# Optimization experiments

Measured on AMD Instinct MI355X. Metric: run time of the kernel, lower is better.

The kernel has to match this reference:

```python
import jax, jax.numpy as jnp
import numpy as np

INPUT_DIM = 512
HIDDEN_DIM = 512
T, B = 512, 128


def setup_inputs() -> dict:
    key = jax.random.key(0)
    ks = jax.random.split(key, 9)
    s_in = 1.0 / np.sqrt(INPUT_DIM + HIDDEN_DIM)
    d = INPUT_DIM + HIDDEN_DIM
    inputs = jax.random.normal(ks[0], (T, B, INPUT_DIM), dtype=jnp.float32)
    def lin(kw, kb):
        W = jax.random.uniform(kw, (HIDDEN_DIM, d), minval=-s_in, maxval=s_in, dtype=jnp.float32)
        b = jax.random.uniform(kb, (HIDDEN_DIM,), minval=-s_in, maxval=s_in, dtype=jnp.float32)
        return W, b
    Wf, bf = lin(ks[1], ks[2])
    Wi, bi = lin(ks[3], ks[4])
    Wg, bg = lin(ks[5], ks[6])
    Wo, bo = lin(ks[7], ks[8])
    return {"inputs": inputs, "Wf": Wf, "bf": bf, "Wi": Wi, "bi": bi,
            "Wg": Wg, "bg": bg, "Wo": Wo, "bo": bo}


def _lstm(inputs, Wf, bf, Wi, bi, Wg, bg, Wo, bo):
    B_ = inputs.shape[1]
    h0 = jnp.zeros((B_, HIDDEN_DIM), dtype=inputs.dtype)
    c0 = jnp.zeros((B_, HIDDEN_DIM), dtype=inputs.dtype)

    def step(carry, x):
        hx, cx = carry
        combined = jnp.concatenate([x, hx], axis=1)  # [B, input+hidden]
        f = jax.nn.sigmoid(combined @ Wf.T + bf)
        i = jax.nn.sigmoid(combined @ Wi.T + bi)
        g = jnp.tanh(combined @ Wg.T + bg)
        o = jax.nn.sigmoid(combined @ Wo.T + bo)
        cx = f * cx + i * g
        hx = o * jnp.tanh(cx)
        return (hx, cx), hx

    (hx, cx), outputs = jax.lax.scan(step, (h0, c0), inputs)
    return outputs, (hx, cx)


def reference(inputs, Wf, bf, Wi, bi, Wg, bg, Wo, bo):
    return _lstm(inputs, Wf, bf, Wi, bi, Wg, bg, Wo, bo)
```

## Files before the change

kernel.cpp:

```cpp
#include <hip/hip_runtime.h>
#include <stdint.h>

#define T_STEPS 512
#define BATCH   128
#define HID     512
#define KTOT    1024

typedef __attribute__((ext_vector_type(8))) short          bf16x8;
typedef __attribute__((ext_vector_type(8))) unsigned short u16x8;
typedef __attribute__((ext_vector_type(4))) float          f32x4;

__device__ inline unsigned short f2bf(float f) {
    union { float f; unsigned u; } x; x.f = f;
    unsigned r = x.u + 0x7FFFu + ((x.u >> 16) & 1u);
    return (unsigned short)(r >> 16);
}

__device__ inline float sigmoidf_(float x) { return 1.f / (1.f + __expf(-x)); }
__device__ inline float tanhf_(float x)    { float e = __expf(2.f * x); return 1.f - 2.f / (e + 1.f); }

__global__ void cast_x_kernel(const float* __restrict__ x, unsigned short* __restrict__ y, int n) {
    int i = (blockIdx.x * blockDim.x + threadIdx.x) * 8;
    if (i >= n) return;
    float4 a = *(const float4*)(x + i);
    float4 b = *(const float4*)(x + i + 4);
    u16x8 v;
    v[0] = f2bf(a.x); v[1] = f2bf(a.y); v[2] = f2bf(a.z); v[3] = f2bf(a.w);
    v[4] = f2bf(b.x); v[5] = f2bf(b.y); v[6] = f2bf(b.z); v[7] = f2bf(b.w);
    *(u16x8*)(y + i) = v;
}

__device__ inline void load_x32(const float* xf, const unsigned short* xbf, int use_xbf,
                                size_t off, uint4& a, uint4& b) {
    if (use_xbf) {
        const uint4* p = (const uint4*)(xbf + off);
        a = p[0]; b = p[1];
    } else {
        const float4* p = (const float4*)(xf + off);
        float4 f0 = p[0], f1 = p[1], f2 = p[2], f3 = p[3];
        u16x8 v;
        v[0] = f2bf(f0.x); v[1] = f2bf(f0.y); v[2] = f2bf(f0.z); v[3] = f2bf(f0.w);
        v[4] = f2bf(f1.x); v[5] = f2bf(f1.y); v[6] = f2bf(f1.z); v[7] = f2bf(f1.w);
        a = *(uint4*)&v;
        u16x8 w;
        w[0] = f2bf(f2.x); w[1] = f2bf(f2.y); w[2] = f2bf(f2.z); w[3] = f2bf(f2.w);
        w[4] = f2bf(f3.x); w[5] = f2bf(f3.y); w[6] = f2bf(f3.z); w[7] = f2bf(f3.w);
        b = *(uint4*)&w;
    }
}

__global__ __launch_bounds__(512, 2) void lstm_kernel(
    const float* __restrict__ xf,
    const unsigned short* __restrict__ xbf,
    const float* __restrict__ Wf, const float* __restrict__ bfv,
    const float* __restrict__ Wi, const float* __restrict__ biv,
    const float* __restrict__ Wg, const float* __restrict__ bgv,
    const float* __restrict__ Wo, const float* __restrict__ bov,
    float* __restrict__ out,
    unsigned int* __restrict__ flags,
    unsigned short* __restrict__ hbuf,
    int use_xbf)
{
    __shared__ __align__(16) unsigned short comb[16][1048];
    __shared__ float gp[4][4][16][34];

    const int tid  = threadIdx.x;
    const int bgc  = blockIdx.x >> 4;
    const int cg   = blockIdx.x & 15;
    const int w    = tid >> 6;
    const int lane = tid & 63;
    const int kh   = w & 3;
    const int uh   = w >> 2;
    const int n    = lane & 15;
    const int quad = lane >> 4;
    const int unit = cg * 32 + uh * 16 + n;

    bf16x8 wfr[4][8];
    {
        const float* Wptr[4] = {Wf, Wi, Wg, Wo};
#pragma unroll
        for (int g = 0; g < 4; ++g) {
            const float* wrow = Wptr[g] + (size_t)unit * KTOT;
#pragma unroll
            for (int j = 0; j < 8; ++j) {
                const int kk = (j < 4) ? (kh * 4 + j) : (16 + kh * 4 + (j - 4));
                const float4* p = (const float4*)(wrow + kk * 32 + quad * 8);
                float4 a = p[0], b = p[1];
                u16x8 v;
                v[0] = f2bf(a.x); v[1] = f2bf(a.y); v[2] = f2bf(a.z); v[3] = f2bf(a.w);
                v[4] = f2bf(b.x); v[5] = f2bf(b.y); v[6] = f2bf(b.z); v[7] = f2bf(b.w);
                wfr[g][j] = (bf16x8)v;
            }
        }
    }

    const int srow = tid >> 5;
    const int scol = tid & 31;

    const int bc = srow, uc = scol;
    float creg = 0.f;
    const int bglob = bgc * 16 + bc;
    const int uglob = cg * 32 + uc;
    const int bgrow = bgc * 16 + srow;

    float biasv[4];
    biasv[0] = bfv[uglob]; biasv[1] = biv[uglob];
    biasv[2] = bgv[uglob]; biasv[3] = bov[uglob];

    const size_t xstride = (size_t)HID;

    {
        uint4 a, b;
        load_x32(xf, xbf, use_xbf, ((size_t)(0 * BATCH + bgrow)) * xstride + scol * 16, a, b);
        *(uint4*)&comb[srow][scol * 16]     = a;
        *(uint4*)&comb[srow][scol * 16 + 8] = b;
        uint4 z = {0u, 0u, 0u, 0u};
        *(uint4*)&comb[srow][512 + scol * 16]     = z;
        *(uint4*)&comb[srow][512 + scol * 16 + 8] = z;
    }
    __syncthreads();

    f32x4 acc[4];
#pragma unroll
    for (int g = 0; g < 4; ++g) acc[g] = (f32x4){0.f, 0.f, 0.f, 0.f};
    {
        bf16x8 af[4];
#pragma unroll
        for (int j = 0; j < 4; ++j)
            af[j] = *(const bf16x8*)&comb[n][(kh * 4 + j) * 32 + quad * 8];
#pragma unroll
        for (int j = 0; j < 4; ++j)
#pragma unroll
            for (int g = 0; g < 4; ++g)
                acc[g] = __builtin_amdgcn_mfma_f32_16x16x32_bf16(af[j], wfr[g][j], acc[g], 0, 0, 0);
    }

    uint4 pfa, pfb;
    load_x32(xf, xbf, use_xbf, ((size_t)(1 * BATCH + bgrow)) * xstride + scol * 16, pfa, pfb);

    for (int t = 0; t < T_STEPS; ++t) {
        if (t > 0) {
            if (lane < 16) {
                unsigned int* fp = flags + ((size_t)(t - 1) * 8 + bgc) * 16 + lane;
                while (__hip_atomic_load(fp, __ATOMIC_RELAXED, __HIP_MEMORY_SCOPE_AGENT) == 0u) {}
            }
            const unsigned long long* src = (const unsigned long long*)
                (hbuf + (size_t)((t - 1) & 1) * BATCH * HID + (size_t)bgrow * HID + scol * 16);
            unsigned long long v0 = __hip_atomic_load(src + 0, __ATOMIC_RELAXED, __HIP_MEMORY_SCOPE_AGENT);
            unsigned long long v1 = __hip_atomic_load(src + 1, __ATOMIC_RELAXED, __HIP_MEMORY_SCOPE_AGENT);
            unsigned long long v2 = __hip_atomic_load(src + 2, __ATOMIC_RELAXED, __HIP_MEMORY_SCOPE_AGENT);
            unsigned long long v3 = __hip_atomic_load(src + 3, __ATOMIC_RELAXED, __HIP_MEMORY_SCOPE_AGENT);
            uint4 a, b;
            a.x = (unsigned)v0; a.y = (unsigned)(v0 >> 32);
            a.z = (unsigned)v1; a.w = (unsigned)(v1 >> 32);
            b.x = (unsigned)v2; b.y = (unsigned)(v2 >> 32);
            b.z = (unsigned)v3; b.w = (unsigned)(v3 >> 32);
            *(uint4*)&comb[srow][512 + scol * 16]     = a;
            *(uint4*)&comb[srow][512 + scol * 16 + 8] = b;
        }
        __syncthreads();

        {
            bf16x8 af[4];
#pragma unroll
            for (int j = 0; j < 4; ++j)
                af[j] = *(const bf16x8*)&comb[n][(16 + kh * 4 + j) * 32 + quad * 8];
#pragma unroll
            for (int j = 0; j < 4; ++j)
#pragma unroll
                for (int g = 0; g < 4; ++g)
                    acc[g] = __builtin_amdgcn_mfma_f32_16x16x32_bf16(af[j], wfr[g][4 + j], acc[g], 0, 0, 0);
        }

#pragma unroll
        for (int g = 0; g < 4; ++g)
#pragma unroll
            for (int r = 0; r < 4; ++r)
                gp[kh][g][quad * 4 + r][uh * 16 + n] = acc[g][r];
        if (t + 1 < T_STEPS) {
            *(uint4*)&comb[srow][scol * 16]     = pfa;
            *(uint4*)&comb[srow][scol * 16 + 8] = pfb;
        }
        __syncthreads();

        {
            float s0 = gp[0][0][bc][uc] + gp[1][0][bc][uc] + gp[2][0][bc][uc] + gp[3][0][bc][uc] + biasv[0];
            float s1 = gp[0][1][bc][uc] + gp[1][1][bc][uc] + gp[2][1][bc][uc] + gp[3][1][bc][uc] + biasv[1];
            float s2 = gp[0][2][bc][uc] + gp[1][2][bc][uc] + gp[2][2][bc][uc] + gp[3][2][bc][uc] + biasv[2];
            float s3 = gp[0][3][bc][uc] + gp[1][3][bc][uc] + gp[2][3][bc][uc] + gp[3][3][bc][uc] + biasv[3];
            float fv = sigmoidf_(s0);
            float iv = sigmoidf_(s1);
            float gv = tanhf_(s2);
            float ov = sigmoidf_(s3);
            float cn = fv * creg + iv * gv;
            creg = cn;
            float hv = ov * tanhf_(cn);
            unsigned int us  = (unsigned int)f2bf(hv);
            unsigned int us1 = (unsigned int)__shfl_down((int)us, 1);
            if ((uc & 1) == 0) {
                unsigned int pv = us | (us1 << 16);
                unsigned int* hp = (unsigned int*)(hbuf + (size_t)(t & 1) * BATCH * HID
                                                   + (size_t)bglob * HID + uglob);
                __hip_atomic_store(hp, pv, __ATOMIC_RELAXED, __HIP_MEMORY_SCOPE_AGENT);
            }
            out[(size_t)t * BATCH * HID + (size_t)bglob * HID + uglob] = hv;
            if (t == T_STEPS - 1) {
                out[(size_t)T_STEPS * BATCH * HID + (size_t)bglob * HID + uglob] = hv;
                out[(size_t)T_STEPS * BATCH * HID + BATCH * HID + (size_t)bglob * HID + uglob] = cn;
            }
        }

        if (t + 1 < T_STEPS) {
#pragma unroll
            for (int g = 0; g < 4; ++g) acc[g] = (f32x4){0.f, 0.f, 0.f, 0.f};
            bf16x8 af[4];
#pragma unroll
            for (int j = 0; j < 4; ++j)
                af[j] = *(const bf16x8*)&comb[n][(kh * 4 + j) * 32 + quad * 8];
#pragma unroll
            for (int j = 0; j < 4; ++j)
#pragma unroll
                for (int g = 0; g < 4; ++g)
                    acc[g] = __builtin_amdgcn_mfma_f32_16x16x32_bf16(af[j], wfr[g][j], acc[g], 0, 0, 0);
        }

        __builtin_amdgcn_s_waitcnt(0);
        __syncthreads();
        if (tid == 0) {
            __hip_atomic_store(flags + ((size_t)t * 8 + bgc) * 16 + cg, 1u,
                               __ATOMIC_RELAXED, __HIP_MEMORY_SCOPE_AGENT);
        }
        if (t + 2 < T_STEPS) {
            load_x32(xf, xbf, use_xbf,
                     ((size_t)((t + 2) * BATCH + bgrow)) * xstride + scol * 16, pfa, pfb);
        }
    }
}

extern "C" void kernel_launch(void* const* d_in, const int* in_sizes, int n_in,
                              void* d_out, int out_size, void* d_ws, size_t ws_size,
                              hipStream_t stream) {
    (void)in_sizes; (void)n_in; (void)out_size;
    const float* x   = (const float*)d_in[0];
    const float* Wf  = (const float*)d_in[1];
    const float* bfv = (const float*)d_in[2];
    const float* Wi  = (const float*)d_in[3];
    const float* biv = (const float*)d_in[4];
    const float* Wg  = (const float*)d_in[5];
    const float* bgv = (const float*)d_in[6];
    const float* Wo  = (const float*)d_in[7];
    const float* bov = (const float*)d_in[8];
    float* out = (float*)d_out;

    unsigned char* ws = (unsigned char*)d_ws;
    unsigned int*   flags = (unsigned int*)ws;
    unsigned short* hbuf  = (unsigned short*)(ws + 262144);
    unsigned short* xbf   = (unsigned short*)(ws + 524288);

    size_t need = 524288 + (size_t)T_STEPS * BATCH * HID * 2;
    int use_xbf = (ws_size >= need) ? 1 : 0;

    hipMemsetAsync(flags, 0, 262144, stream);
    if (use_xbf) {
        int nelem = T_STEPS * BATCH * HID;
        cast_x_kernel<<<nelem / (256 * 8), 256, 0, stream>>>(x, xbf, nelem);
    }
    lstm_kernel<<<dim3(128), dim3(512), 0, stream>>>(
        x, xbf, Wf, bfv, Wi, biv, Wg, bgv, Wo, bov, out, flags, hbuf, use_xbf);
}
```

Baseline: 1.899 ms.

## Load h directly into MFMA registers with per-wave flags, double-buffer LDS

Each wave now loads its slice of the previous hidden state from global memory straight into MFMA operand registers instead of staging it through shared memory. It waits only on the 32 per-wave flags covering that slice rather than on per-block flags. The x and gate-partial LDS buffers are double-buffered, which removes one block barrier per step, and each wave signals its own flag without a trailing block-wide sync. Output stores move after the flag signal so they leave the critical path. The cost is more flag polling traffic, each lane reading more h from global memory, and a larger flag array to clear.

```diff
diff --git a/kernel.cpp b/kernel.cpp
--- a/kernel.cpp
+++ b/kernel.cpp
@@ -61,8 +61,8 @@
     unsigned short* __restrict__ hbuf,
     int use_xbf)
 {
-    __shared__ __align__(16) unsigned short comb[16][1048];
-    __shared__ float gp[4][4][16][34];
+    __shared__ __align__(16) unsigned short xbuf[2][16][520];
+    __shared__ float gp[2][4][4][16][34];
 
     const int tid  = threadIdx.x;
     const int bgc  = blockIdx.x >> 4;
@@ -112,11 +112,8 @@
     {
         uint4 a, b;
         load_x32(xf, xbf, use_xbf, ((size_t)(0 * BATCH + bgrow)) * xstride + scol * 16, a, b);
-        *(uint4*)&comb[srow][scol * 16]     = a;
-        *(uint4*)&comb[srow][scol * 16 + 8] = b;
-        uint4 z = {0u, 0u, 0u, 0u};
-        *(uint4*)&comb[srow][512 + scol * 16]     = z;
-        *(uint4*)&comb[srow][512 + scol * 16 + 8] = z;
+        *(uint4*)&xbuf[0][srow][scol * 16]     = a;
+        *(uint4*)&xbuf[0][srow][scol * 16 + 8] = b;
     }
     __syncthreads();
 
@@ -127,7 +124,7 @@
         bf16x8 af[4];
 #pragma unroll
         for (int j = 0; j < 4; ++j)
-            af[j] = *(const bf16x8*)&comb[n][(kh * 4 + j) * 32 + quad * 8];
+            af[j] = *(const bf16x8*)&xbuf[0][n][(kh * 4 + j) * 32 + quad * 8];
 #pragma unroll
         for (int j = 0; j < 4; ++j)
 #pragma unroll
@@ -140,74 +137,75 @@
 
     for (int t = 0; t < T_STEPS; ++t) {
         if (t > 0) {
-            if (lane < 16) {
-                unsigned int* fp = flags + ((size_t)(t - 1) * 8 + bgc) * 16 + lane;
+            if (lane < 32) {
+                const unsigned int* fp = flags + ((size_t)(t - 1) * 8 + bgc) * 128 + kh * 32 + lane;
                 while (__hip_atomic_load(fp, __ATOMIC_RELAXED, __HIP_MEMORY_SCOPE_AGENT) == 0u) {}
             }
-            const unsigned long long* src = (const unsigned long long*)
-                (hbuf + (size_t)((t - 1) & 1) * BATCH * HID + (size_t)bgrow * HID + scol * 16);
-            unsigned long long v0 = __hip_atomic_load(src + 0, __ATOMIC_RELAXED, __HIP_MEMORY_SCOPE_AGENT);
-            unsigned long long v1 = __hip_atomic_load(src + 1, __ATOMIC_RELAXED, __HIP_MEMORY_SCOPE_AGENT);
-            unsigned long long v2 = __hip_atomic_load(src + 2, __ATOMIC_RELAXED, __HIP_MEMORY_SCOPE_AGENT);
-            unsigned long long v3 = __hip_atomic_load(src + 3, __ATOMIC_RELAXED, __HIP_MEMORY_SCOPE_AGENT);
-            uint4 a, b;
-            a.x = (unsigned)v0; a.y = (unsigned)(v0 >> 32);
-            a.z = (unsigned)v1; a.w = (unsigned)(v1 >> 32);
-            b.x = (unsigned)v2; b.y = (unsigned)(v2 >> 32);
-            b.z = (unsigned)v3; b.w = (unsigned)(v3 >> 32);
-            *(uint4*)&comb[srow][512 + scol * 16]     = a;
-            *(uint4*)&comb[srow][512 + scol * 16 + 8] = b;
+            const unsigned short* hb = hbuf + (size_t)((t - 1) & 1) * BATCH * HID
+                                     + (size_t)(bgc * 16 + n) * HID + kh * 128 + quad * 8;
+            unsigned long long q0 = __hip_atomic_load((const unsigned long long*)(hb + 0),       __ATOMIC_RELAXED, __HIP_MEMORY_SCOPE_AGENT);
+            unsigned long long q1 = __hip_atomic_load((const unsigned long long*)(hb + 4),       __ATOMIC_RELAXED, __HIP_MEMORY_SCOPE_AGENT);
+            unsigned long long q2 = __hip_atomic_load((const unsigned long long*)(hb + 32),      __ATOMIC_RELAXED, __HIP_MEMORY_SCOPE_AGENT);
+            unsigned long long q3 = __hip_atomic_load((const unsigned long long*)(hb + 36),      __ATOMIC_RELAXED, __HIP_MEMORY_SCOPE_AGENT);
+            unsigned long long q4 = __hip_atomic_load((const unsigned long long*)(hb + 64),      __ATOMIC_RELAXED, __HIP_MEMORY_SCOPE_AGENT);
+            unsigned long long q5 = __hip_atomic_load((const unsigned long long*)(hb + 68),      __ATOMIC_RELAXED, __HIP_MEMORY_SCOPE_AGENT);
+            unsigned long long q6 = __hip_atomic_load((const unsigned long long*)(hb + 96),      __ATOMIC_RELAXED, __HIP_MEMORY_SCOPE_AGENT);
+            unsigned long long q7 = __hip_atomic_load((const unsigned long long*)(hb + 100),     __ATOMIC_RELAXED, __HIP_MEMORY_SCOPE_AGENT);
+            bf16x8 haf[4];
+            {
+                uint4 u;
+                u.x = (unsigned)q0; u.y = (unsigned)(q0 >> 32);
+                u.z = (unsigned)q1; u.w = (unsigned)(q1 >> 32);
+                haf[0] = *(bf16x8*)&u;
+                u.x = (unsigned)q2; u.y = (unsigned)(q2 >> 32);
+                u.z = (unsigned)q3; u.w = (unsigned)(q3 >> 32);
+                haf[1] = *(bf16x8*)&u;
+                u.x = (unsigned)q4; u.y = (unsigned)(q4 >> 32);
+                u.z = (unsigned)q5; u.w = (unsigned)(q5 >> 32);
+                haf[2] = *(bf16x8*)&u;
+                u.x = (unsigned)q6; u.y = (unsigned)(q6 >> 32);
+                u.z = (unsigned)q7; u.w = (unsigned)(q7 >> 32);
+                haf[3] = *(bf16x8*)&u;
+            }
+#pragma unroll
+            for (int j = 0; j < 4; ++j)
+#pragma unroll
+                for (int g = 0; g < 4; ++g)
+                    acc[g] = __builtin_amdgcn_mfma_f32_16x16x32_bf16(haf[j], wfr[g][4 + j], acc[g], 0, 0, 0);
+        }
+
+#pragma unroll
+        for (int g = 0; g < 4; ++g)
+#pragma unroll
+            for (int r = 0; r < 4; ++r)
+                gp[t & 1][kh][g][quad * 4 + r][uh * 16 + n] = acc[g][r];
+        if (t + 1 < T_STEPS) {
+            *(uint4*)&xbuf[(t + 1) & 1][srow][scol * 16]     = pfa;
+            *(uint4*)&xbuf[(t + 1) & 1][srow][scol * 16 + 8] = pfb;
         }
         __syncthreads();
 
+        float hv, cn;
         {
-            bf16x8 af[4];
-#pragma unroll
-            for (int j = 0; j < 4; ++j)
-                af[j] = *(const bf16x8*)&comb[n][(16 + kh * 4 + j) * 32 + quad * 8];
-#pragma unroll
-            for (int j = 0; j < 4; ++j)
-#pragma unroll
-                for (int g = 0; g < 4; ++g)
-                    acc[g] = __builtin_amdgcn_mfma_f32_16x16x32_bf16(af[j], wfr[g][4 + j], acc[g], 0, 0, 0);
-        }
-
-#pragma unroll
-        for (int g = 0; g < 4; ++g)
-#pragma unroll
-            for (int r = 0; r < 4; ++r)
-                gp[kh][g][quad * 4 + r][uh * 16 + n] = acc[g][r];
-        if (t + 1 < T_STEPS) {
-            *(uint4*)&comb[srow][scol * 16]     = pfa;
-            *(uint4*)&comb[srow][scol * 16 + 8] = pfb;
-        }
-        __syncthreads();
-
-        {
-            float s0 = gp[0][0][bc][uc] + gp[1][0][bc][uc] + gp[2][0][bc][uc] + gp[3][0][bc][uc] + biasv[0];
-            float s1 = gp[0][1][bc][uc] + gp[1][1][bc][uc] + gp[2][1][bc][uc] + gp[3][1][bc][uc] + biasv[1];
-            float s2 = gp[0][2][bc][uc] + gp[1][2][bc][uc] + gp[2][2][bc][uc] + gp[3][2][bc][uc] + biasv[2];
-            float s3 = gp[0][3][bc][uc] + gp[1][3][bc][uc] + gp[2][3][bc][uc] + gp[3][3][bc][uc] + biasv[3];
+            float s0 = gp[t & 1][0][0][bc][uc] + gp[t & 1][1][0][bc][uc] + gp[t & 1][2][0][bc][uc] + gp[t & 1][3][0][bc][uc] + biasv[0];
+            float s1 = gp[t & 1][0][1][bc][uc] + gp[t & 1][1][1][bc][uc] + gp[t & 1][2][1][bc][uc] + gp[t & 1][3][1][bc][uc] + biasv[1];
+            float s2 = gp[t & 1][0][2][bc][uc] + gp[t & 1][1][2][bc][uc] + gp[t & 1][2][2][bc][uc] + gp[t & 1][3][2][bc][uc] + biasv[2];
+            float s3 = gp[t & 1][0][3][bc][uc] + gp[t & 1][1][3][bc][uc] + gp[t & 1][2][3][bc][uc] + gp[t & 1][3][3][bc][uc] + biasv[3];
             float fv = sigmoidf_(s0);
             float iv = sigmoidf_(s1);
             float gv = tanhf_(s2);
             float ov = sigmoidf_(s3);
-            float cn = fv * creg + iv * gv;
+            cn = fv * creg + iv * gv;
             creg = cn;
-            float hv = ov * tanhf_(cn);
+            hv = ov * tanhf_(cn);
             unsigned int us  = (unsigned int)f2bf(hv);
             unsigned int us1 = (unsigned int)__shfl_down((int)us, 1);
-            if ((uc & 1) == 0) {
+            if (t + 1 < T_STEPS && (uc & 1) == 0) {
                 unsigned int pv = us | (us1 << 16);
                 unsigned int* hp = (unsigned int*)(hbuf + (size_t)(t & 1) * BATCH * HID
                                                    + (size_t)bglob * HID + uglob);
                 __hip_atomic_store(hp, pv, __ATOMIC_RELAXED, __HIP_MEMORY_SCOPE_AGENT);
             }
-            out[(size_t)t * BATCH * HID + (size_t)bglob * HID + uglob] = hv;
-            if (t == T_STEPS - 1) {
-                out[(size_t)T_STEPS * BATCH * HID + (size_t)bglob * HID + uglob] = hv;
-                out[(size_t)T_STEPS * BATCH * HID + BATCH * HID + (size_t)bglob * HID + uglob] = cn;
-            }
         }
 
         if (t + 1 < T_STEPS) {
@@ -216,7 +214,7 @@
             bf16x8 af[4];
 #pragma unroll
             for (int j = 0; j < 4; ++j)
-                af[j] = *(const bf16x8*)&comb[n][(kh * 4 + j) * 32 + quad * 8];
+                af[j] = *(const bf16x8*)&xbuf[(t + 1) & 1][n][(kh * 4 + j) * 32 + quad * 8];
 #pragma unroll
             for (int j = 0; j < 4; ++j)
 #pragma unroll
@@ -225,10 +223,15 @@
         }
 
         __builtin_amdgcn_s_waitcnt(0);
-        __syncthreads();
-        if (tid == 0) {
-            __hip_atomic_store(flags + ((size_t)t * 8 + bgc) * 16 + cg, 1u,
+        if (lane == 0 && t + 1 < T_STEPS) {
+            __hip_atomic_store(flags + ((size_t)t * 8 + bgc) * 128 + cg * 8 + w, 1u,
                                __ATOMIC_RELAXED, __HIP_MEMORY_SCOPE_AGENT);
+        }
+
+        out[(size_t)t * BATCH * HID + (size_t)bglob * HID + uglob] = hv;
+        if (t == T_STEPS - 1) {
+            out[(size_t)T_STEPS * BATCH * HID + (size_t)bglob * HID + uglob] = hv;
+            out[(size_t)T_STEPS * BATCH * HID + BATCH * HID + (size_t)bglob * HID + uglob] = cn;
         }
         if (t + 2 < T_STEPS) {
             load_x32(xf, xbf, use_xbf,
@@ -254,13 +257,13 @@
 
     unsigned char* ws = (unsigned char*)d_ws;
     unsigned int*   flags = (unsigned int*)ws;
-    unsigned short* hbuf  = (unsigned short*)(ws + 262144);
-    unsigned short* xbf   = (unsigned short*)(ws + 524288);
-
-    size_t need = 524288 + (size_t)T_STEPS * BATCH * HID * 2;
+    unsigned short* hbuf  = (unsigned short*)(ws + 2097152);
+    unsigned short* xbf   = (unsigned short*)(ws + 2359296);
+
+    size_t need = 2359296 + (size_t)T_STEPS * BATCH * HID * 2;
     int use_xbf = (ws_size >= need) ? 1 : 0;
 
-    hipMemsetAsync(flags, 0, 262144, stream);
+    hipMemsetAsync(flags, 0, 2097152, stream);
     if (use_xbf) {
         int nelem = T_STEPS * BATCH * HID;
         cast_x_kernel<<<nelem / (256 * 8), 256, 0, stream>>>(x, xbf, nelem);
```

Result: slower. 2.702 ms (+42.3%).
